# Optimization experiments

Hardware: AMD Instinct MI355X
Metric: run time of the kernel (lower is better)

## Reference

```python
import jax, jax.numpy as jnp
import numpy as np

H = 64
NG = 100000   # gene nodes
ND = 30000    # disease nodes
NE = 1500000  # gda edges (gene -> disease)
NL = 500000   # supervision (label) edges


def setup_inputs() -> dict:
    key = jax.random.key(0)
    ks = jax.random.split(key, 20)
    s = 0.1
    inp = {
        "gene_emb":    jax.random.normal(ks[0], (NG, H), jnp.float32) * s,
        "disease_emb": jax.random.normal(ks[1], (ND, H), jnp.float32) * s,
    }
    wnames = ["w1_gd_l", "w1_gd_r", "w1_dg_l", "w1_dg_r",
              "w2_gd_l", "w2_gd_r", "w2_dg_l", "w2_dg_r"]
    for i, n in enumerate(wnames):
        inp[n] = jax.random.normal(ks[2 + i], (H, H), jnp.float32) * s
    for i, n in enumerate(["b1_gd", "b1_dg", "b2_gd", "b2_dg"]):
        inp[n] = jax.random.normal(ks[10 + i], (H,), jnp.float32) * 0.01
    inp["edge_src"]  = jax.random.randint(ks[14], (NE,), 0, NG)
    inp["edge_dst"]  = jax.random.randint(ks[15], (NE,), 0, ND)
    inp["label_src"] = jax.random.randint(ks[16], (NL,), 0, NG)
    inp["label_dst"] = jax.random.randint(ks[17], (NL,), 0, ND)
    return inp


def _sage(x_src, x_dst, src, dst, n_dst, wl, wr, b):
    # SAGEConv (mean aggr): lin_l(mean_{j in N(i)} x_j) + lin_r(x_i) + b
    msum = jax.ops.segment_sum(x_src[src], dst, num_segments=n_dst)
    cnt = jax.ops.segment_sum(jnp.ones((src.shape[0], 1), x_src.dtype), dst,
                              num_segments=n_dst)
    mean = msum / jnp.maximum(cnt, 1.0)
    return mean @ wl + x_dst @ wr + b


def reference(gene_emb, disease_emb,
              w1_gd_l, w1_gd_r, b1_gd, w1_dg_l, w1_dg_r, b1_dg,
              w2_gd_l, w2_gd_r, b2_gd, w2_dg_l, w2_dg_r, b2_dg,
              edge_src, edge_dst, label_src, label_dst):
    # layer 1 (hetero: gene->disease via gda, disease->gene via rev_gda)
    h_d = jax.nn.relu(_sage(gene_emb, disease_emb, edge_src, edge_dst, ND,
                            w1_gd_l, w1_gd_r, b1_gd))
    h_g = jax.nn.relu(_sage(disease_emb, gene_emb, edge_dst, edge_src, NG,
                            w1_dg_l, w1_dg_r, b1_dg))
    # layer 2 (no activation)
    h_d2 = _sage(h_g, h_d, edge_src, edge_dst, ND, w2_gd_l, w2_gd_r, b2_gd)
    h_g2 = _sage(h_d, h_g, edge_dst, edge_src, NG, w2_dg_l, w2_dg_r, b2_dg)
    # classifier: dot product over label edges
    return jnp.sum(h_g2[label_src] * h_d2[label_dst], axis=-1)
```

## Files before the change

kernel.cpp:

```cpp
#include <hip/hip_runtime.h>
#include <hip/hip_bf16.h>

#define H 64
#define SCAN_CHUNK 512
#define NB1 512

typedef unsigned short u16;
typedef unsigned int u32;
typedef __attribute__((ext_vector_type(8))) __bf16 bf16x8;
typedef __attribute__((ext_vector_type(4))) float f32x4;

__device__ __forceinline__ float bflo(u32 u) {
    return __builtin_bit_cast(float, u << 16);
}
__device__ __forceinline__ float bfhi(u32 u) {
    return __builtin_bit_cast(float, u & 0xffff0000u);
}
__device__ __forceinline__ u16 bf16rne(float f) {
    u32 u = __builtin_bit_cast(u32, f);
    return (u16)((u + 0x7FFFu + ((u >> 16) & 1u)) >> 16);
}

__global__ __launch_bounds__(256) void fused_count_convert_kernel(
    const int* __restrict__ es, const int* __restrict__ ed,
    int* __restrict__ histD, int* __restrict__ histG,
    int ne, int shiftD, int shiftG,
    const float* __restrict__ a, u16* __restrict__ oa, long long na4,
    const float* __restrict__ b, u16* __restrict__ ob, long long nb4)
{
    if (blockIdx.x < NB1) {
        __shared__ int lhd[256], lhg[256];
        const int tid = threadIdx.x;
        lhd[tid] = 0; lhg[tid] = 0;
        __syncthreads();
        const int chunk = (ne + NB1 - 1) / NB1;
        const int e0 = blockIdx.x * chunk;
        const int e1 = min(e0 + chunk, ne);
        for (int e = e0 + tid; e < e1; e += 256) {
            atomicAdd(&lhd[ed[e] >> shiftD], 1);
            atomicAdd(&lhg[es[e] >> shiftG], 1);
        }
        __syncthreads();
        histD[tid * NB1 + blockIdx.x] = lhd[tid];
        histG[tid * NB1 + blockIdx.x] = lhg[tid];
        return;
    }
    long long i = (long long)(blockIdx.x - NB1) * 256 + threadIdx.x;
    const float* src; u16* dst; long long q;
    if (i < na4) { src = a; dst = oa; q = i; }
    else if (i < na4 + nb4) { src = b; dst = ob; q = i - na4; }
    else return;
    float4 v = *(const float4*)&src[q * 4];
    ushort4 o;
    o.x = bf16rne(v.x); o.y = bf16rne(v.y);
    o.z = bf16rne(v.z); o.w = bf16rne(v.w);
    *(ushort4*)&dst[q * 4] = o;
}

__global__ __launch_bounds__(256) void scan_reduce_kernel(
    const int* __restrict__ a1, int n1, const int* __restrict__ a2, int n2,
    int B1, int* __restrict__ partial)
{
    const int b = blockIdx.x;
    const int* a; int n, base;
    if (b < B1) { a = a1; n = n1; base = b * SCAN_CHUNK; }
    else        { a = a2; n = n2; base = (b - B1) * SCAN_CHUNK; }
    int t = threadIdx.x;
    int i0 = base + 2 * t, i1 = i0 + 1;
    int v = ((i0 < n) ? a[i0] : 0) + ((i1 < n) ? a[i1] : 0);
    #pragma unroll
    for (int off = 32; off > 0; off >>= 1) v += __shfl_down(v, off, 64);
    __shared__ int ws[4];
    if ((t & 63) == 0) ws[t >> 6] = v;
    __syncthreads();
    if (t == 0) partial[b] = ws[0] + ws[1] + ws[2] + ws[3];
}

__global__ __launch_bounds__(1024) void scan_partials_kernel(
    const int* __restrict__ partial, int* __restrict__ blockOff,
    int B1, int nbtot,
    int* __restrict__ out1, int n1, int* __restrict__ out2, int n2)
{
    __shared__ int sA[1024], sB[1024];
    int t = threadIdx.x;
    int x = (t < nbtot) ? partial[t] : 0;
    sA[t] = x;
    __syncthreads();
    int* cur = sA; int* nxt = sB;
    for (int off = 1; off < 1024; off <<= 1) {
        int v = cur[t];
        if (t >= off) v += cur[t - off];
        nxt[t] = v;
        __syncthreads();
        int* tmp = cur; cur = nxt; nxt = tmp;
    }
    int incl = cur[t];
    int excl = incl - x;
    int tot1 = cur[B1 - 1];
    if (t < nbtot) blockOff[t] = excl - ((t >= B1) ? tot1 : 0);
    if (t == 0) out1[n1] = tot1;
    if (t == nbtot - 1) out2[n2] = incl - tot1;
}

__global__ __launch_bounds__(256) void scan_apply_kernel(
    const int* __restrict__ a1, int* __restrict__ out1, int n1,
    const int* __restrict__ a2, int* __restrict__ out2, int n2,
    int B1, const int* __restrict__ blockOff)
{
    const int b = blockIdx.x;
    const int* a; int* out; int n, base;
    if (b < B1) { a = a1; out = out1; n = n1; base = b * SCAN_CHUNK; }
    else        { a = a2; out = out2; n = n2; base = (b - B1) * SCAN_CHUNK; }
    int t = threadIdx.x;
    int lane = t & 63, wid = t >> 6;
    int i0 = base + 2 * t, i1 = i0 + 1;
    int x0 = (i0 < n) ? a[i0] : 0;
    int x1 = (i1 < n) ? a[i1] : 0;
    int p = x0 + x1;
    int P = p;
    #pragma unroll
    for (int off = 1; off < 64; off <<= 1) {
        int u = __shfl_up(P, off, 64);
        if (lane >= off) P += u;
    }
    __shared__ int ws[4];
    if (lane == 63) ws[wid] = P;
    __syncthreads();
    int waveBase = 0;
    #pragma unroll
    for (int w = 0; w < 4; ++w) waveBase += (w < wid) ? ws[w] : 0;
    int off0 = blockOff[b] + waveBase + (P - p);
    if (i0 < n) out[i0] = off0;
    if (i1 < n) out[i1] = off0 + x0;
}

__global__ __launch_bounds__(256) void part_scatter_kernel(
    const int* __restrict__ es, const int* __restrict__ ed,
    const int* __restrict__ baseD, const int* __restrict__ baseG,
    int2* __restrict__ pairD, int2* __restrict__ pairG,
    int ne, int shiftD, int shiftG)
{
    __shared__ int curD[256], curG[256];
    const int tid = threadIdx.x;
    curD[tid] = baseD[tid * NB1 + blockIdx.x];
    curG[tid] = baseG[tid * NB1 + blockIdx.x];
    __syncthreads();
    const int chunk = (ne + NB1 - 1) / NB1;
    const int e0 = blockIdx.x * chunk;
    const int e1 = min(e0 + chunk, ne);
    for (int e = e0 + tid; e < e1; e += 256) {
        int s = es[e], d = ed[e];
        int pD = atomicAdd(&curD[d >> shiftD], 1);
        pairD[pD] = make_int2(d, s);
        int pG = atomicAdd(&curG[s >> shiftG], 1);
        pairG[pG] = make_int2(s, d);
    }
}

__global__ __launch_bounds__(256) void csr_build_kernel(
    const int2* __restrict__ pairD, const int* __restrict__ baseD,
    int* __restrict__ rowD, int* __restrict__ idxD, int nd, int shiftD, int nbktD,
    const int2* __restrict__ pairG, const int* __restrict__ baseG,
    int* __restrict__ rowG, int* __restrict__ idxG, int ng, int shiftG, int nbktG)
{
    __shared__ int lcnt[512], lcur[512];
    __shared__ int ws[4];
    const int j = blockIdx.x & 255;
    const int isG = blockIdx.x >> 8;
    const int2* pair; const int* base; int* row; int* idx; int n, shift, nbkt;
    if (isG) { pair = pairG; base = baseG; row = rowG; idx = idxG; n = ng; shift = shiftG; nbkt = nbktG; }
    else     { pair = pairD; base = baseD; row = rowD; idx = idxD; n = nd; shift = shiftD; nbkt = nbktD; }
    if (j >= nbkt) return;

    const int tid = threadIdx.x;
    const int nLo = j << shift;
    const int nHi = min(nLo + (1 << shift), n);
    const int range = nHi - nLo;
    const int segBase = base[j * NB1];
    const int segEnd  = base[(j + 1) * NB1];

    lcnt[tid] = 0; lcnt[tid + 256] = 0;
    __syncthreads();
    for (int t = segBase + tid; t < segEnd; t += 256)
        atomicAdd(&lcnt[pair[t].x - nLo], 1);
    __syncthreads();

    int i0 = 2 * tid, i1 = i0 + 1;
    int c0 = (i0 < range) ? lcnt[i0] : 0;
    int c1 = (i1 < range) ? lcnt[i1] : 0;
    int p = c0 + c1;
    int P = p;
    const int lane = tid & 63, wid = tid >> 6;
    #pragma unroll
    for (int off = 1; off < 64; off <<= 1) {
        int u = __shfl_up(P, off, 64);
        if (lane >= off) P += u;
    }
    if (lane == 63) ws[wid] = P;
    __syncthreads();
    int waveBase = 0;
    #pragma unroll
    for (int w = 0; w < 4; ++w) waveBase += (w < wid) ? ws[w] : 0;
    int o0 = segBase + waveBase + (P - p);
    int o1 = o0 + c0;
    if (i0 < range) { row[nLo + i0] = o0; lcur[i0] = o0; }
    if (i1 < range) { row[nLo + i1] = o1; lcur[i1] = o1; }
    if (nHi == n && tid == 0) row[n] = segEnd;
    __syncthreads();

    for (int t = segBase + tid; t < segEnd; t += 256) {
        int2 pr = pair[t];
        int pos = atomicAdd(&lcur[pr.x - nLo], 1);
        idx[pos] = pr.y;
    }
}

__global__ __launch_bounds__(256) void gather_mean_kernel(
    const u16* __restrict__ srcD, const u16* __restrict__ srcG,
    const int* __restrict__ rowD, const int* __restrict__ idxD,
    const int* __restrict__ rowG, const int* __restrict__ idxG,
    u16* __restrict__ outD, u16* __restrict__ outG, int nd, int ng)
{
    int hw = blockIdx.x * 8 + (threadIdx.x >> 5);
    int l5 = threadIdx.x & 31;
    const u16* src; const int* row; const int* idx; u16* out; int node;
    if (hw < nd)            { src = srcD; row = rowD; idx = idxD; out = outD; node = hw; }
    else if (hw < nd + ng)  { src = srcG; row = rowG; idx = idxG; out = outG; node = hw - nd; }
    else return;

    const int sub = l5 >> 3;
    const int c8 = l5 & 7;
    int beg = row[node], end = row[node + 1];

    float a0[8], a1[8];
    #pragma unroll
    for (int j = 0; j < 8; ++j) { a0[j] = 0.f; a1[j] = 0.f; }

    int i = beg;
    for (; i + 8 <= end; i += 8) {
        int s0 = idx[i + sub];
        int s1 = idx[i + 4 + sub];
        uint4 v0 = *((const uint4*)(src + (size_t)s0 * H) + c8);
        uint4 v1 = *((const uint4*)(src + (size_t)s1 * H) + c8);
        a0[0] += bflo(v0.x); a0[1] += bfhi(v0.x); a0[2] += bflo(v0.y); a0[3] += bfhi(v0.y);
        a0[4] += bflo(v0.z); a0[5] += bfhi(v0.z); a0[6] += bflo(v0.w); a0[7] += bfhi(v0.w);
        a1[0] += bflo(v1.x); a1[1] += bfhi(v1.x); a1[2] += bflo(v1.y); a1[3] += bfhi(v1.y);
        a1[4] += bflo(v1.z); a1[5] += bfhi(v1.z); a1[6] += bflo(v1.w); a1[7] += bfhi(v1.w);
    }
    if (i + 4 <= end) {
        int s0 = idx[i + sub];
        uint4 v0 = *((const uint4*)(src + (size_t)s0 * H) + c8);
        a0[0] += bflo(v0.x); a0[1] += bfhi(v0.x); a0[2] += bflo(v0.y); a0[3] += bfhi(v0.y);
        a0[4] += bflo(v0.z); a0[5] += bfhi(v0.z); a0[6] += bflo(v0.w); a0[7] += bfhi(v0.w);
        i += 4;
    }
    if (i + sub < end) {
        int s1 = idx[i + sub];
        uint4 v1 = *((const uint4*)(src + (size_t)s1 * H) + c8);
        a1[0] += bflo(v1.x); a1[1] += bfhi(v1.x); a1[2] += bflo(v1.y); a1[3] += bfhi(v1.y);
        a1[4] += bflo(v1.z); a1[5] += bfhi(v1.z); a1[6] += bflo(v1.w); a1[7] += bfhi(v1.w);
    }
    float acc[8];
    #pragma unroll
    for (int j = 0; j < 8; ++j) acc[j] = a0[j] + a1[j];
    #pragma unroll
    for (int j = 0; j < 8; ++j) {
        acc[j] += __shfl_xor(acc[j], 8, 64);
        acc[j] += __shfl_xor(acc[j], 16, 64);
    }
    if (sub == 0) {
        float inv = 1.0f / fmaxf((float)(end - beg), 1.0f);
        u32 w0 = (u32)bf16rne(acc[0] * inv) | ((u32)bf16rne(acc[1] * inv) << 16);
        u32 w1 = (u32)bf16rne(acc[2] * inv) | ((u32)bf16rne(acc[3] * inv) << 16);
        u32 w2 = (u32)bf16rne(acc[4] * inv) | ((u32)bf16rne(acc[5] * inv) << 16);
        u32 w3 = (u32)bf16rne(acc[6] * inv) | ((u32)bf16rne(acc[7] * inv) << 16);
        uint4 pk = make_uint4(w0, w1, w2, w3);
        *(uint4*)(out + (size_t)node * H + c8 * 8) = pk;
    }
}

template <bool RELU>
__global__ __launch_bounds__(256) void sage_mm_mfma_kernel(
    const u16* __restrict__ meanD, const u16* __restrict__ xD, u16* __restrict__ outD,
    const float* __restrict__ wlD, const float* __restrict__ wrD,
    const float* __restrict__ bD, int nd,
    const u16* __restrict__ meanG, const u16* __restrict__ xG, u16* __restrict__ outG,
    const float* __restrict__ wlG, const float* __restrict__ wrG,
    const float* __restrict__ bG, int ng, int MBD)
{
    __shared__ u16 sB[16 * 64 * 8];
    int b = blockIdx.x;
    const u16 *mean, *x; u16* out; const float *wl, *wr, *bias; int n;
    if (b < MBD) { mean = meanD; x = xD; out = outD; wl = wlD; wr = wrD; bias = bD; n = nd; }
    else { b -= MBD; mean = meanG; x = xG; out = outG; wl = wlG; wr = wrG; bias = bG; n = ng; }

    const int tid = threadIdx.x;
    for (int i = tid; i < 4096; i += 256) {
        int k = i >> 6, ncol = i & 63;
        int q = (k >> 3) & 3, j = k & 7, t = ncol >> 4, n15 = ncol & 15;
        int lane = q * 16 + n15;
        int c0 = k >> 5;
        sB[(((c0 + 0) * 4 + t) * 64 + lane) * 8 + j] = bf16rne(wl[i]);
        sB[(((c0 + 2) * 4 + t) * 64 + lane) * 8 + j] = bf16rne(wr[i]);
    }
    __syncthreads();

    const int lane = tid & 63;
    const int wave = tid >> 6;
    const int m = lane & 15;
    const int q = lane >> 4;

    bf16x8 Bf[16];
    {
        const uint4* sB4 = (const uint4*)sB;
        #pragma unroll
        for (int f = 0; f < 16; ++f)
            Bf[f] = __builtin_bit_cast(bf16x8, sB4[f * 64 + lane]);
    }
    float bv[4];
    #pragma unroll
    for (int t = 0; t < 4; ++t) bv[t] = bias[t * 16 + m];

    const int row0 = b * 256;
    #pragma unroll
    for (int r = 0; r < 4; ++r) {
        int rbase = row0 + (wave + 4 * r) * 16;
        if (rbase >= n) break;
        int gr = min(rbase + m, n - 1);
        const uint4* mrow = (const uint4*)(mean + (size_t)gr * H);
        const uint4* xrow = (const uint4*)(x + (size_t)gr * H);
        bf16x8 A0 = __builtin_bit_cast(bf16x8, mrow[q]);
        bf16x8 A1 = __builtin_bit_cast(bf16x8, mrow[q + 4]);
        bf16x8 A2 = __builtin_bit_cast(bf16x8, xrow[q]);
        bf16x8 A3 = __builtin_bit_cast(bf16x8, xrow[q + 4]);
        f32x4 acc[4];
        #pragma unroll
        for (int t = 0; t < 4; ++t) acc[t] = (f32x4){bv[t], bv[t], bv[t], bv[t]};
        #pragma unroll
        for (int t = 0; t < 4; ++t) {
            acc[t] = __builtin_amdgcn_mfma_f32_16x16x32_bf16(A0, Bf[0 * 4 + t], acc[t], 0, 0, 0);
            acc[t] = __builtin_amdgcn_mfma_f32_16x16x32_bf16(A1, Bf[1 * 4 + t], acc[t], 0, 0, 0);
            acc[t] = __builtin_amdgcn_mfma_f32_16x16x32_bf16(A2, Bf[2 * 4 + t], acc[t], 0, 0, 0);
            acc[t] = __builtin_amdgcn_mfma_f32_16x16x32_bf16(A3, Bf[3 * 4 + t], acc[t], 0, 0, 0);
        }
        #pragma unroll
        for (int reg = 0; reg < 4; ++reg) {
            int orow = rbase + q * 4 + reg;
            if (orow < n) {
                u16* op = out + (size_t)orow * H;
                #pragma unroll
                for (int t = 0; t < 4; ++t) {
                    float v = acc[t][reg];
                    if (RELU) v = fmaxf(v, 0.0f);
                    op[t * 16 + m] = bf16rne(v);
                }
            }
        }
    }
}

__global__ __launch_bounds__(256) void classify_kernel(
    const u16* __restrict__ hg2, const u16* __restrict__ hd2,
    const int* __restrict__ ls, const int* __restrict__ ld,
    float* __restrict__ out, int nl)
{
    long long t = (long long)blockIdx.x * blockDim.x + threadIdx.x;
    int e = (int)(t >> 3);
    int c8 = (int)(t & 7);
    if (e >= nl) return;
    int a = ls[e];
    int b = ld[e];
    uint4 ua = *((const uint4*)(hg2 + (size_t)a * H) + c8);
    uint4 ub = *((const uint4*)(hd2 + (size_t)b * H) + c8);
    float v = bflo(ua.x) * bflo(ub.x) + bfhi(ua.x) * bfhi(ub.x)
            + bflo(ua.y) * bflo(ub.y) + bfhi(ua.y) * bfhi(ub.y)
            + bflo(ua.z) * bflo(ub.z) + bfhi(ua.z) * bfhi(ub.z)
            + bflo(ua.w) * bflo(ub.w) + bfhi(ua.w) * bfhi(ub.w);
    v += __shfl_xor(v, 1, 64);
    v += __shfl_xor(v, 2, 64);
    v += __shfl_xor(v, 4, 64);
    if (c8 == 0) out[e] = v;
}

extern "C" void kernel_launch(void* const* d_in, const int* in_sizes, int n_in,
                              void* d_out, int out_size, void* d_ws, size_t ws_size,
                              hipStream_t stream)
{
    const float* gene  = (const float*)d_in[0];
    const float* dis   = (const float*)d_in[1];
    const float* w1gdl = (const float*)d_in[2];
    const float* w1gdr = (const float*)d_in[3];
    const float* w1dgl = (const float*)d_in[4];
    const float* w1dgr = (const float*)d_in[5];
    const float* w2gdl = (const float*)d_in[6];
    const float* w2gdr = (const float*)d_in[7];
    const float* w2dgl = (const float*)d_in[8];
    const float* w2dgr = (const float*)d_in[9];
    const float* b1gd  = (const float*)d_in[10];
    const float* b1dg  = (const float*)d_in[11];
    const float* b2gd  = (const float*)d_in[12];
    const float* b2dg  = (const float*)d_in[13];
    const int* es = (const int*)d_in[14];
    const int* ed = (const int*)d_in[15];
    const int* ls = (const int*)d_in[16];
    const int* ld = (const int*)d_in[17];

    const int ng = in_sizes[0] / H;
    const int nd = in_sizes[1] / H;
    const int ne = in_sizes[14];
    const int nl = in_sizes[16];

    int shiftD = 0; while (((nd + (1 << shiftD) - 1) >> shiftD) > 256) ++shiftD;
    int shiftG = 0; while (((ng + (1 << shiftG) - 1) >> shiftG) > 256) ++shiftG;
    const int nbktD = (nd + (1 << shiftD) - 1) >> shiftD;
    const int nbktG = (ng + (1 << shiftG) - 1) >> shiftG;
    const int n1 = 256 * NB1;

    int* rowD = (int*)d_ws;
    int* rowG = rowD + nd + 1;
    int* idxD = rowG + ng + 1;
    int* idxG = idxD + ne;
    u16* geneBf = (u16*)(idxG + ne);
    u16* disBf  = geneBf + (size_t)ng * H;
    u16* h1Dbf  = disBf + (size_t)nd * H;
    u16* h1Gbf  = h1Dbf + (size_t)nd * H;
    u16* h2Dbf  = h1Gbf + (size_t)ng * H;
    u16* h2Gbf  = h2Dbf + (size_t)nd * H;
    uintptr_t p = (uintptr_t)(h2Gbf + (size_t)ng * H);
    p = (p + 15) & ~(uintptr_t)15;
    u16* MD = (u16*)p;
    u16* MG = MD + (size_t)nd * H;
    int* histD = (int*)p;
    int* histG = histD + n1;
    int* baseD = histG + n1;
    int* baseG = baseD + n1 + 1;
    int* partial  = baseG + n1 + 1;
    int* blockOff = partial + 1024;
    uintptr_t pp = (uintptr_t)(blockOff + 1024);
    pp = (pp + 15) & ~(uintptr_t)15;
    int2* pairD = (int2*)pp;
    int2* pairG = pairD + ne;

    const long long na4 = (long long)ng * H / 4;
    const long long nb4 = (long long)nd * H / 4;
    const int convBlocks = (int)((na4 + nb4 + 255) / 256);
    fused_count_convert_kernel<<<NB1 + convBlocks, 256, 0, stream>>>(
        es, ed, histD, histG, ne, shiftD, shiftG,
        gene, geneBf, na4, dis, disBf, nb4);

    const int B1 = n1 / SCAN_CHUNK;
    const int nbtot = 2 * B1;
    scan_reduce_kernel<<<nbtot, 256, 0, stream>>>(histD, n1, histG, n1, B1, partial);
    scan_partials_kernel<<<1, 1024, 0, stream>>>(partial, blockOff, B1, nbtot,
                                                 baseD, n1, baseG, n1);
    scan_apply_kernel<<<nbtot, 256, 0, stream>>>(histD, baseD, n1,
                                                 histG, baseG, n1, B1, blockOff);
    part_scatter_kernel<<<NB1, 256, 0, stream>>>(es, ed, baseD, baseG,
                                                 pairD, pairG, ne, shiftD, shiftG);
    csr_build_kernel<<<512, 256, 0, stream>>>(
        pairD, baseD, rowD, idxD, nd, shiftD, nbktD,
        pairG, baseG, rowG, idxG, ng, shiftG, nbktG);

    const int gatherBlocks = (nd + ng + 7) / 8;
    const int MBD = (nd + 255) / 256;
    const int MBG = (ng + 255) / 256;

    gather_mean_kernel<<<gatherBlocks, 256, 0, stream>>>(
        geneBf, disBf, rowD, idxD, rowG, idxG, MD, MG, nd, ng);
    sage_mm_mfma_kernel<true><<<MBD + MBG, 256, 0, stream>>>(
        MD, disBf, h1Dbf, w1gdl, w1gdr, b1gd, nd,
        MG, geneBf, h1Gbf, w1dgl, w1dgr, b1dg, ng, MBD);

    gather_mean_kernel<<<gatherBlocks, 256, 0, stream>>>(
        h1Gbf, h1Dbf, rowD, idxD, rowG, idxG, MD, MG, nd, ng);
    sage_mm_mfma_kernel<false><<<MBD + MBG, 256, 0, stream>>>(
        MD, h1Dbf, h2Dbf, w2gdl, w2gdr, b2gd, nd,
        MG, h1Gbf, h2Gbf, w2dgl, w2dgr, b2dg, ng, MBD);

    {
        long long threads = (long long)nl * 8;
        int blocks = (int)((threads + 255) / 256);
        classify_kernel<<<blocks, 256, 0, stream>>>(h2Gbf, h2Dbf, ls, ld,
                                                    (float*)d_out, nl);
    }
}
```

Measured before the change: 372.1 us.

## Fold partial scan into apply, pack CSR pairs to 32-bit, unroll gather

```diff
diff --git a/kernel.cpp b/kernel.cpp
--- a/kernel.cpp
+++ b/kernel.cpp
@@ -76,60 +76,69 @@
     if (t == 0) partial[b] = ws[0] + ws[1] + ws[2] + ws[3];
 }
 
-__global__ __launch_bounds__(1024) void scan_partials_kernel(
-    const int* __restrict__ partial, int* __restrict__ blockOff,
-    int B1, int nbtot,
-    int* __restrict__ out1, int n1, int* __restrict__ out2, int n2)
-{
-    __shared__ int sA[1024], sB[1024];
-    int t = threadIdx.x;
-    int x = (t < nbtot) ? partial[t] : 0;
-    sA[t] = x;
-    __syncthreads();
-    int* cur = sA; int* nxt = sB;
-    for (int off = 1; off < 1024; off <<= 1) {
-        int v = cur[t];
-        if (t >= off) v += cur[t - off];
-        nxt[t] = v;
-        __syncthreads();
-        int* tmp = cur; cur = nxt; nxt = tmp;
-    }
-    int incl = cur[t];
-    int excl = incl - x;
-    int tot1 = cur[B1 - 1];
-    if (t < nbtot) blockOff[t] = excl - ((t >= B1) ? tot1 : 0);
-    if (t == 0) out1[n1] = tot1;
-    if (t == nbtot - 1) out2[n2] = incl - tot1;
-}
-
 __global__ __launch_bounds__(256) void scan_apply_kernel(
     const int* __restrict__ a1, int* __restrict__ out1, int n1,
     const int* __restrict__ a2, int* __restrict__ out2, int n2,
-    int B1, const int* __restrict__ blockOff)
-{
+    int B1, int nbtot, const int* __restrict__ partial)
+{
+    __shared__ int sExcl[1024];
+    __shared__ int ws[4];
+    const int tid = threadIdx.x;
+    const int lane = tid & 63, wid = tid >> 6;
+
+    int j0 = 4 * tid;
+    int p0 = (j0 + 0 < nbtot) ? partial[j0 + 0] : 0;
+    int p1 = (j0 + 1 < nbtot) ? partial[j0 + 1] : 0;
+    int p2 = (j0 + 2 < nbtot) ? partial[j0 + 2] : 0;
+    int p3 = (j0 + 3 < nbtot) ? partial[j0 + 3] : 0;
+    int psum = p0 + p1 + p2 + p3;
+    int P = psum;
+    #pragma unroll
+    for (int off = 1; off < 64; off <<= 1) {
+        int u = __shfl_up(P, off, 64);
+        if (lane >= off) P += u;
+    }
+    if (lane == 63) ws[wid] = P;
+    __syncthreads();
+    int wbase = 0;
+    #pragma unroll
+    for (int w = 0; w < 4; ++w) wbase += (w < wid) ? ws[w] : 0;
+    int e = wbase + (P - psum);
+    sExcl[j0 + 0] = e;
+    sExcl[j0 + 1] = e + p0;
+    sExcl[j0 + 2] = e + p0 + p1;
+    sExcl[j0 + 3] = e + p0 + p1 + p2;
+    __syncthreads();
+
     const int b = blockIdx.x;
+    int tot1 = sExcl[B1 - 1] + ((B1 - 1 < nbtot) ? partial[B1 - 1] : 0);
+    int myOff = sExcl[b] - ((b >= B1) ? tot1 : 0);
+    if (b == 0 && tid == 0) {
+        int tot2 = sExcl[nbtot - 1] + partial[nbtot - 1] - tot1;
+        out1[n1] = tot1;
+        out2[n2] = tot2;
+    }
+    __syncthreads();
+
     const int* a; int* out; int n, base;
     if (b < B1) { a = a1; out = out1; n = n1; base = b * SCAN_CHUNK; }
     else        { a = a2; out = out2; n = n2; base = (b - B1) * SCAN_CHUNK; }
-    int t = threadIdx.x;
-    int lane = t & 63, wid = t >> 6;
-    int i0 = base + 2 * t, i1 = i0 + 1;
+    int i0 = base + 2 * tid, i1 = i0 + 1;
     int x0 = (i0 < n) ? a[i0] : 0;
     int x1 = (i1 < n) ? a[i1] : 0;
     int p = x0 + x1;
-    int P = p;
+    int Q = p;
     #pragma unroll
     for (int off = 1; off < 64; off <<= 1) {
-        int u = __shfl_up(P, off, 64);
-        if (lane >= off) P += u;
-    }
-    __shared__ int ws[4];
-    if (lane == 63) ws[wid] = P;
+        int u = __shfl_up(Q, off, 64);
+        if (lane >= off) Q += u;
+    }
+    if (lane == 63) ws[wid] = Q;
     __syncthreads();
     int waveBase = 0;
     #pragma unroll
     for (int w = 0; w < 4; ++w) waveBase += (w < wid) ? ws[w] : 0;
-    int off0 = blockOff[b] + waveBase + (P - p);
+    int off0 = myOff + waveBase + (Q - p);
     if (i0 < n) out[i0] = off0;
     if (i1 < n) out[i1] = off0 + x0;
 }
@@ -137,7 +146,7 @@
 __global__ __launch_bounds__(256) void part_scatter_kernel(
     const int* __restrict__ es, const int* __restrict__ ed,
     const int* __restrict__ baseD, const int* __restrict__ baseG,
-    int2* __restrict__ pairD, int2* __restrict__ pairG,
+    u32* __restrict__ pairD, u32* __restrict__ pairG,
     int ne, int shiftD, int shiftG)
 {
     __shared__ int curD[256], curG[256];
@@ -145,29 +154,31 @@
     curD[tid] = baseD[tid * NB1 + blockIdx.x];
     curG[tid] = baseG[tid * NB1 + blockIdx.x];
     __syncthreads();
+    const int maskD = (1 << shiftD) - 1;
+    const int maskG = (1 << shiftG) - 1;
     const int chunk = (ne + NB1 - 1) / NB1;
     const int e0 = blockIdx.x * chunk;
     const int e1 = min(e0 + chunk, ne);
     for (int e = e0 + tid; e < e1; e += 256) {
         int s = es[e], d = ed[e];
         int pD = atomicAdd(&curD[d >> shiftD], 1);
-        pairD[pD] = make_int2(d, s);
+        pairD[pD] = ((u32)(d & maskD) << 17) | (u32)s;
         int pG = atomicAdd(&curG[s >> shiftG], 1);
-        pairG[pG] = make_int2(s, d);
+        pairG[pG] = ((u32)(s & maskG) << 17) | (u32)d;
     }
 }
 
 __global__ __launch_bounds__(256) void csr_build_kernel(
-    const int2* __restrict__ pairD, const int* __restrict__ baseD,
+    const u32* __restrict__ pairD, const int* __restrict__ baseD,
     int* __restrict__ rowD, int* __restrict__ idxD, int nd, int shiftD, int nbktD,
-    const int2* __restrict__ pairG, const int* __restrict__ baseG,
+    const u32* __restrict__ pairG, const int* __restrict__ baseG,
     int* __restrict__ rowG, int* __restrict__ idxG, int ng, int shiftG, int nbktG)
 {
     __shared__ int lcnt[512], lcur[512];
     __shared__ int ws[4];
     const int j = blockIdx.x & 255;
     const int isG = blockIdx.x >> 8;
-    const int2* pair; const int* base; int* row; int* idx; int n, shift, nbkt;
+    const u32* pair; const int* base; int* row; int* idx; int n, shift, nbkt;
     if (isG) { pair = pairG; base = baseG; row = rowG; idx = idxG; n = ng; shift = shiftG; nbkt = nbktG; }
     else     { pair = pairD; base = baseD; row = rowD; idx = idxD; n = nd; shift = shiftD; nbkt = nbktD; }
     if (j >= nbkt) return;
@@ -182,7 +193,7 @@
     lcnt[tid] = 0; lcnt[tid + 256] = 0;
     __syncthreads();
     for (int t = segBase + tid; t < segEnd; t += 256)
-        atomicAdd(&lcnt[pair[t].x - nLo], 1);
+        atomicAdd(&lcnt[pair[t] >> 17], 1);
     __syncthreads();
 
     int i0 = 2 * tid, i1 = i0 + 1;
@@ -209,9 +220,9 @@
     __syncthreads();
 
     for (int t = segBase + tid; t < segEnd; t += 256) {
-        int2 pr = pair[t];
-        int pos = atomicAdd(&lcur[pr.x - nLo], 1);
-        idx[pos] = pr.y;
+        u32 pr = pair[t];
+        int pos = atomicAdd(&lcur[pr >> 17], 1);
+        idx[pos] = (int)(pr & 0x1FFFFu);
     }
 }
 
@@ -232,12 +243,30 @@
     const int c8 = l5 & 7;
     int beg = row[node], end = row[node + 1];
 
-    float a0[8], a1[8];
-    #pragma unroll
-    for (int j = 0; j < 8; ++j) { a0[j] = 0.f; a1[j] = 0.f; }
+    float a0[8], a1[8], a2[8], a3[8];
+    #pragma unroll
+    for (int j = 0; j < 8; ++j) { a0[j] = 0.f; a1[j] = 0.f; a2[j] = 0.f; a3[j] = 0.f; }
 
     int i = beg;
-    for (; i + 8 <= end; i += 8) {
+    for (; i + 16 <= end; i += 16) {
+        int s0 = idx[i + sub];
+        int s1 = idx[i + 4 + sub];
+        int s2 = idx[i + 8 + sub];
+        int s3 = idx[i + 12 + sub];
+        uint4 v0 = *((const uint4*)(src + (size_t)s0 * H) + c8);
+        uint4 v1 = *((const uint4*)(src + (size_t)s1 * H) + c8);
+        uint4 v2 = *((const uint4*)(src + (size_t)s2 * H) + c8);
+        uint4 v3 = *((const uint4*)(src + (size_t)s3 * H) + c8);
+        a0[0] += bflo(v0.x); a0[1] += bfhi(v0.x); a0[2] += bflo(v0.y); a0[3] += bfhi(v0.y);
+        a0[4] += bflo(v0.z); a0[5] += bfhi(v0.z); a0[6] += bflo(v0.w); a0[7] += bfhi(v0.w);
+        a1[0] += bflo(v1.x); a1[1] += bfhi(v1.x); a1[2] += bflo(v1.y); a1[3] += bfhi(v1.y);
+        a1[4] += bflo(v1.z); a1[5] += bfhi(v1.z); a1[6] += bflo(v1.w); a1[7] += bfhi(v1.w);
+        a2[0] += bflo(v2.x); a2[1] += bfhi(v2.x); a2[2] += bflo(v2.y); a2[3] += bfhi(v2.y);
+        a2[4] += bflo(v2.z); a2[5] += bfhi(v2.z); a2[6] += bflo(v2.w); a2[7] += bfhi(v2.w);
+        a3[0] += bflo(v3.x); a3[1] += bfhi(v3.x); a3[2] += bflo(v3.y); a3[3] += bfhi(v3.y);
+        a3[4] += bflo(v3.z); a3[5] += bfhi(v3.z); a3[6] += bflo(v3.w); a3[7] += bfhi(v3.w);
+    }
+    if (i + 8 <= end) {
         int s0 = idx[i + sub];
         int s1 = idx[i + 4 + sub];
         uint4 v0 = *((const uint4*)(src + (size_t)s0 * H) + c8);
@@ -246,23 +275,24 @@
         a0[4] += bflo(v0.z); a0[5] += bfhi(v0.z); a0[6] += bflo(v0.w); a0[7] += bfhi(v0.w);
         a1[0] += bflo(v1.x); a1[1] += bfhi(v1.x); a1[2] += bflo(v1.y); a1[3] += bfhi(v1.y);
         a1[4] += bflo(v1.z); a1[5] += bfhi(v1.z); a1[6] += bflo(v1.w); a1[7] += bfhi(v1.w);
+        i += 8;
     }
     if (i + 4 <= end) {
         int s0 = idx[i + sub];
         uint4 v0 = *((const uint4*)(src + (size_t)s0 * H) + c8);
-        a0[0] += bflo(v0.x); a0[1] += bfhi(v0.x); a0[2] += bflo(v0.y); a0[3] += bfhi(v0.y);
-        a0[4] += bflo(v0.z); a0[5] += bfhi(v0.z); a0[6] += bflo(v0.w); a0[7] += bfhi(v0.w);
+        a2[0] += bflo(v0.x); a2[1] += bfhi(v0.x); a2[2] += bflo(v0.y); a2[3] += bfhi(v0.y);
+        a2[4] += bflo(v0.z); a2[5] += bfhi(v0.z); a2[6] += bflo(v0.w); a2[7] += bfhi(v0.w);
         i += 4;
     }
     if (i + sub < end) {
         int s1 = idx[i + sub];
         uint4 v1 = *((const uint4*)(src + (size_t)s1 * H) + c8);
-        a1[0] += bflo(v1.x); a1[1] += bfhi(v1.x); a1[2] += bflo(v1.y); a1[3] += bfhi(v1.y);
-        a1[4] += bflo(v1.z); a1[5] += bfhi(v1.z); a1[6] += bflo(v1.w); a1[7] += bfhi(v1.w);
+        a3[0] += bflo(v1.x); a3[1] += bfhi(v1.x); a3[2] += bflo(v1.y); a3[3] += bfhi(v1.y);
+        a3[4] += bflo(v1.z); a3[5] += bfhi(v1.z); a3[6] += bflo(v1.w); a3[7] += bfhi(v1.w);
     }
     float acc[8];
     #pragma unroll
-    for (int j = 0; j < 8; ++j) acc[j] = a0[j] + a1[j];
+    for (int j = 0; j < 8; ++j) acc[j] = (a0[j] + a1[j]) + (a2[j] + a3[j]);
     #pragma unroll
     for (int j = 0; j < 8; ++j) {
         acc[j] += __shfl_xor(acc[j], 8, 64);
@@ -435,11 +465,10 @@
     int* baseD = histG + n1;
     int* baseG = baseD + n1 + 1;
     int* partial  = baseG + n1 + 1;
-    int* blockOff = partial + 1024;
-    uintptr_t pp = (uintptr_t)(blockOff + 1024);
+    uintptr_t pp = (uintptr_t)(partial + 1024);
     pp = (pp + 15) & ~(uintptr_t)15;
-    int2* pairD = (int2*)pp;
-    int2* pairG = pairD + ne;
+    u32* pairD = (u32*)pp;
+    u32* pairG = pairD + ne;
 
     const long long na4 = (long long)ng * H / 4;
     const long long nb4 = (long long)nd * H / 4;
@@ -451,10 +480,9 @@
     const int B1 = n1 / SCAN_CHUNK;
     const int nbtot = 2 * B1;
     scan_reduce_kernel<<<nbtot, 256, 0, stream>>>(histD, n1, histG, n1, B1, partial);
-    scan_partials_kernel<<<1, 1024, 0, stream>>>(partial, blockOff, B1, nbtot,
-                                                 baseD, n1, baseG, n1);
     scan_apply_kernel<<<nbtot, 256, 0, stream>>>(histD, baseD, n1,
-                                                 histG, baseG, n1, B1, blockOff);
+                                                 histG, baseG, n1, B1, nbtot, partial);
+
     part_scatter_kernel<<<NB1, 256, 0, stream>>>(es, ed, baseD, baseG,
                                                  pairD, pairG, ne, shiftD, shiftG);
     csr_build_kernel<<<512, 256, 0, stream>>>(
```

Result: no change. 376.8 us (+1.3%).
